# Kernel tuning notes

Measured on AMD Instinct MI355X. Metric: run time of the kernel, lower is better.

Reference implementation:

```python
import jax, jax.numpy as jnp
import numpy as np

XBOUND = (-51.2, 51.2, 0.8)
YBOUND = (-51.2, 51.2, 0.8)
ZBOUND = (-10.0, 10.0, 20.0)
DBOUND = (1.0, 60.0, 1.0)
IMG_H, IMG_W = 256, 704
DOWNSAMPLE = 16
CAM_C = 64
OUT_C = 64
D = int((DBOUND[1] - DBOUND[0]) / DBOUND[2])      # 59
NX = int((XBOUND[1] - XBOUND[0]) / XBOUND[2])     # 128
NY = int((YBOUND[1] - YBOUND[0]) / YBOUND[2])     # 128
NZ = int((ZBOUND[1] - ZBOUND[0]) / ZBOUND[2])     # 1
FH, FW = IMG_H // DOWNSAMPLE, IMG_W // DOWNSAMPLE # 16, 44
DX = jnp.array([XBOUND[2], YBOUND[2], ZBOUND[2]], dtype=jnp.float32)
BX = jnp.array([XBOUND[0] + XBOUND[2] / 2.0, YBOUND[0] + YBOUND[2] / 2.0, ZBOUND[0] + ZBOUND[2] / 2.0], dtype=jnp.float32)


def make_frustum():
    ds = jnp.arange(DBOUND[0], DBOUND[1], DBOUND[2], dtype=jnp.float32)   # [D]
    xs = jnp.linspace(0.0, IMG_W - 1.0, FW, dtype=jnp.float32)            # [FW]
    ys = jnp.linspace(0.0, IMG_H - 1.0, FH, dtype=jnp.float32)            # [FH]
    d = jnp.broadcast_to(ds[:, None, None], (D, FH, FW))
    x = jnp.broadcast_to(xs[None, None, :], (D, FH, FW))
    y = jnp.broadcast_to(ys[None, :, None], (D, FH, FW))
    return jnp.stack([x, y, d], axis=-1)                                  # [D,FH,FW,3]


def get_geometry(rots, trans, intrins, post_rots, post_trans):
    # rots/intrins/post_rots: [B,N,3,3]; trans/post_trans: [B,N,3]
    frustum = make_frustum()                                              # [D,FH,FW,3]
    pts = frustum[None, None] - post_trans[:, :, None, None, None]        # [B,N,D,FH,FW,3]
    pts = jnp.einsum('bnij,bndhwj->bndhwi', jnp.linalg.inv(post_rots), pts)
    pts = jnp.concatenate([pts[..., :2] * pts[..., 2:3], pts[..., 2:3]], axis=-1)
    comb = jnp.matmul(rots, jnp.linalg.inv(intrins))
    pts = jnp.einsum('bnij,bndhwj->bndhwi', comb, pts)
    return pts + trans[:, :, None, None, None]


def forward(x, rots, trans, intrins, post_rots, post_trans, w_depth, b_depth):
    B, N, C_in, H, W = x.shape
    # 1x1 conv == channel matmul
    y = jnp.einsum('bnchw,oc->bnohw', x, w_depth) + b_depth[None, None, :, None, None]
    depth = jax.nn.softmax(y[:, :, :D], axis=2)              # [B,N,D,H,W]
    context = y[:, :, D:]                                    # [B,N,OUT_C,H,W]
    outer = depth[:, :, :, None] * context[:, :, None, :]    # [B,N,D,OUT_C,H,W]
    outer = jnp.transpose(outer, (0, 1, 2, 4, 5, 3))         # [B,N,D,H,W,OUT_C]

    geom = jax.lax.stop_gradient(get_geometry(rots, trans, intrins, post_rots, post_trans))
    # torch .long() truncates toward zero -> jnp.trunc
    g = jnp.trunc((geom.reshape(-1, 3) - (BX - DX / 2.0)) / DX).astype(jnp.int32)  # [P,3]
    kept = ((g[:, 0] >= 0) & (g[:, 0] < NX) &
            (g[:, 1] >= 0) & (g[:, 1] < NY) &
            (g[:, 2] >= 0) & (g[:, 2] < NZ))
    batch_ix = jnp.repeat(jnp.arange(B, dtype=jnp.int32), N * D * H * W)
    ranks = batch_ix * (NX * NY * NZ) + g[:, 0] + g[:, 1] * NX + g[:, 2] * NX * NY
    # segment-sum over voxel ranks == sort+cumsum trick + scatter in the original
    feats = jnp.where(kept[:, None], outer.reshape(-1, OUT_C), 0.0)
    ranks = jnp.where(kept, ranks, 0)
    bev = jax.ops.segment_sum(feats, ranks, num_segments=B * NZ * NY * NX)
    bev = bev.reshape(B, NZ, NY, NX, OUT_C).transpose(0, 4, 1, 2, 3).sum(axis=2)
    return bev  # [B, OUT_C, NY, NX]


def setup_inputs() -> dict:
    key = jax.random.key(0)
    B, N = 4, 6
    ks = jax.random.split(key, 8)
    cam2ego = jnp.array([[0.0, 0.0, 1.0], [-1.0, 0.0, 0.0], [0.0, -1.0, 0.0]], dtype=jnp.float32)
    rots = jnp.broadcast_to(cam2ego, (B, N, 3, 3)) + 0.02 * jax.random.normal(ks[0], (B, N, 3, 3), dtype=jnp.float32)
    trans = 1.0 * jax.random.normal(ks[1], (B, N, 3), dtype=jnp.float32)
    K = jnp.array([[700.0, 0.0, IMG_W / 2.0], [0.0, 700.0, IMG_H / 2.0], [0.0, 0.0, 1.0]], dtype=jnp.float32)
    intrins = jnp.broadcast_to(K, (B, N, 3, 3)) + 0.1 * jax.random.normal(ks[2], (B, N, 3, 3), dtype=jnp.float32)
    post_rots = jnp.broadcast_to(jnp.eye(3, dtype=jnp.float32), (B, N, 3, 3)) + 0.01 * jax.random.normal(ks[3], (B, N, 3, 3), dtype=jnp.float32)
    post_trans = 0.1 * jax.random.normal(ks[4], (B, N, 3), dtype=jnp.float32)
    x = jax.random.normal(ks[5], (B, N, CAM_C, FH, FW), dtype=jnp.float32)
    w_depth = 0.05 * jax.random.normal(ks[6], (D + OUT_C, CAM_C), dtype=jnp.float32)
    b_depth = jnp.zeros((D + OUT_C,), dtype=jnp.float32)
    return {"x": x, "rots": rots, "trans": trans, "intrins": intrins,
            "post_rots": post_rots, "post_trans": post_trans,
            "w_depth": w_depth, "b_depth": b_depth}


def reference(x, rots, trans, intrins, post_rots, post_trans, w_depth, b_depth):
    return forward(x, rots, trans, intrins, post_rots, post_trans, w_depth, b_depth)
```

## Files before the change

kernel.cpp:

```cpp
#include <hip/hip_runtime.h>
#include <math.h>

#define Bc 4
#define Nc 6
#define Dc 59
#define FHc 16
#define FWc 44
#define Cc 64
#define OCc 123
#define NXc 128
#define NYc 128
#define NVOX (Bc*NXc*NYc)
#define NBLK (Bc*Nc*FWc)

#define WS_ACC 0
#define WS_CAM ((size_t)16777216)
#define WS_WDT ((size_t)16781312)

template<bool FMA>
__device__ __forceinline__ float mulsub(float a, float b, float c) {
    if (FMA) return __fmaf_rn(-a, b, c);
    return __fadd_rn(c, __fmul_rn(-a, b));
}

template<bool FMA>
__device__ __forceinline__ void lu_inv3x3T(const float* __restrict__ m, float* __restrict__ o) {
    float A[3][3] = {{m[0],m[3],m[6]},{m[1],m[4],m[7]},{m[2],m[5],m[8]}};
    int piv0, piv1;
    {
        float a0=fabsf(A[0][0]), a1=fabsf(A[1][0]), a2=fabsf(A[2][0]);
        int p = 0; float mx = a0;
        if (a1 > mx) { mx = a1; p = 1; }
        if (a2 > mx) { mx = a2; p = 2; }
        piv0 = p;
        if (p != 0) { for (int k=0;k<3;++k){ float t=A[0][k]; A[0][k]=A[p][k]; A[p][k]=t; } }
        const float d = __fdiv_rn(1.0f, A[0][0]);
        A[1][0] = __fmul_rn(A[1][0], d);
        A[2][0] = __fmul_rn(A[2][0], d);
        #pragma unroll
        for (int i=1;i<3;++i)
            #pragma unroll
            for (int j=1;j<3;++j)
                A[i][j] = mulsub<FMA>(A[i][0], A[0][j], A[i][j]);
    }
    {
        float a1=fabsf(A[1][1]), a2=fabsf(A[2][1]);
        int p = (a2 > a1) ? 2 : 1;
        piv1 = p;
        if (p != 1) { for (int k=0;k<3;++k){ float t=A[1][k]; A[1][k]=A[p][k]; A[p][k]=t; } }
        const float d = __fdiv_rn(1.0f, A[1][1]);
        A[2][1] = __fmul_rn(A[2][1], d);
        A[2][2] = mulsub<FMA>(A[2][1], A[1][2], A[2][2]);
    }
    float B[3][3] = {{1.f,0.f,0.f},{0.f,1.f,0.f},{0.f,0.f,1.f}};
    if (piv0 != 0) { for (int k=0;k<3;++k){ float t=B[0][k]; B[0][k]=B[piv0][k]; B[piv0][k]=t; } }
    if (piv1 != 1) { for (int k=0;k<3;++k){ float t=B[1][k]; B[1][k]=B[piv1][k]; B[piv1][k]=t; } }
    #pragma unroll
    for (int j=0;j<3;++j) {
        B[1][j] = mulsub<FMA>(A[1][0], B[0][j], B[1][j]);
        B[2][j] = mulsub<FMA>(A[2][0], B[0][j], B[2][j]);
        B[2][j] = mulsub<FMA>(A[2][1], B[1][j], B[2][j]);
        B[2][j] = __fdiv_rn(B[2][j], A[2][2]);
        B[0][j] = mulsub<FMA>(A[0][2], B[2][j], B[0][j]);
        B[1][j] = mulsub<FMA>(A[1][2], B[2][j], B[1][j]);
        B[1][j] = __fdiv_rn(B[1][j], A[1][1]);
        B[0][j] = mulsub<FMA>(A[0][1], B[1][j], B[0][j]);
        B[0][j] = __fdiv_rn(B[0][j], A[0][0]);
    }
    o[0]=B[0][0]; o[1]=B[1][0]; o[2]=B[2][0];
    o[3]=B[0][1]; o[4]=B[1][1]; o[5]=B[2][1];
    o[6]=B[0][2]; o[7]=B[1][2]; o[8]=B[2][2];
}

template<bool FMA>
__device__ __forceinline__ float dot3(float a0,float a1,float a2,float b0,float b1,float b2){
    if (FMA) return __fmaf_rn(a2,b2, __fmaf_rn(a1,b1, __fmul_rn(a0,b0)));
    return __fadd_rn(__fadd_rn(__fmul_rn(a0,b0), __fmul_rn(a1,b1)), __fmul_rn(a2,b2));
}

__global__ __launch_bounds__(256) void prep(
    const float* __restrict__ wd, const float* __restrict__ rots,
    const float* __restrict__ intrins, const float* __restrict__ post_rots,
    float* __restrict__ wdT2, float* __restrict__ camMat, float4* __restrict__ acc4)
{
    const int gid = blockIdx.x*256 + threadIdx.x;
    const float4 z = make_float4(0.f, 0.f, 0.f, 0.f);
    acc4[gid] = z;
    acc4[gid + 524288] = z;

    if (gid < OCc*Cc) {
        const int o = gid >> 6, c = gid & 63;
        const int slot = (o < 64) ? (o << 1) : (((o - 64) << 1) | 1);
        wdT2[(c << 7) + slot] = wd[gid];
    } else if (gid < OCc*Cc + 320) {
        const int k = gid - OCc*Cc;
        const int c = k / 5, o = 59 + (k % 5);
        wdT2[(c << 7) + (o << 1) + 1] = 0.0f;
    }
    if (gid < 48) {
        const int cam = gid >> 1;
        const int var = gid & 1;
        const float* pr = post_rots + cam*9;
        const float* ro = rots      + cam*9;
        const float* it = intrins   + cam*9;
        float PRi[9], INi[9], CM[9];
        if (var == 0) { lu_inv3x3T<true >(pr, PRi); lu_inv3x3T<true >(it, INi); }
        else          { lu_inv3x3T<false>(pr, PRi); lu_inv3x3T<false>(it, INi); }
        #pragma unroll
        for (int r2 = 0; r2 < 3; ++r2)
            #pragma unroll
            for (int c2 = 0; c2 < 3; ++c2)
                CM[r2*3+c2] = dot3<true>(ro[r2*3+0], ro[r2*3+1], ro[r2*3+2],
                                         INi[0*3+c2], INi[1*3+c2], INi[2*3+c2]);
        float* dst = camMat + (size_t)(cam*2 + var)*18;
        #pragma unroll
        for (int k = 0; k < 9; ++k) { dst[k] = PRi[k]; dst[9+k] = CM[k]; }
    }
}

template<bool FMA>
__device__ __forceinline__ int geom_light(
    const float* __restrict__ PRi, const float* __restrict__ CM,
    float pt0, float pt1, float pt2, float tr0, float tr1, float tr2,
    float u, float v, float dval, int b)
{
    const float p0 = __fsub_rn(u,    pt0);
    const float p1 = __fsub_rn(v,    pt1);
    const float p2 = __fsub_rn(dval, pt2);
    const float q0 = dot3<FMA>(PRi[0],PRi[1],PRi[2], p0,p1,p2);
    const float q1 = dot3<FMA>(PRi[3],PRi[4],PRi[5], p0,p1,p2);
    const float q2 = dot3<FMA>(PRi[6],PRi[7],PRi[8], p0,p1,p2);
    const float r0 = __fmul_rn(q0, q2);
    const float r1 = __fmul_rn(q1, q2);
    const float s0 = __fadd_rn(dot3<FMA>(CM[0],CM[1],CM[2], r0,r1,q2), tr0);
    const float s1 = __fadd_rn(dot3<FMA>(CM[3],CM[4],CM[5], r0,r1,q2), tr1);
    const float s2 = __fadd_rn(dot3<FMA>(CM[6],CM[7],CM[8], r0,r1,q2), tr2);
    const float CX  = -51.200000762939453f;
    const float DXf =  0.80000001192092896f;
    const float gx = __fdiv_rn(__fsub_rn(s0, CX), DXf);
    const float gy = __fdiv_rn(__fsub_rn(s1, CX), DXf);
    const float gz = __fdiv_rn(__fsub_rn(s2, -10.0f), 20.0f);
    const bool kept = (gx > -1.0f) && (gx < 128.0f) &&
                      (gy > -1.0f) && (gy < 128.0f) &&
                      (gz > -1.0f) && (gz < 1.0f);
    return kept ? (b*(NXc*NYc) + ((int)gy)*NXc + (int)gx) : -1;
}

__global__ __launch_bounds__(512, 8) void lss_main(
    const float* __restrict__ x, const float* __restrict__ trans,
    const float* __restrict__ post_trans, const float* __restrict__ bd,
    const float* __restrict__ wdT2, const float* __restrict__ camMat,
    float* __restrict__ acc)
{
    const int blk = blockIdx.x;
    const int wi  = blk % FWc;
    const int cam = blk / FWc;
    const int b   = cam / Nc;
    const int t = threadIdx.x;
    const int wave = t >> 6, lane = t & 63;

    __shared__ float  xsT[64][16];
    __shared__ float  yv[16][60];
    __shared__ float  ctxT[64][18];
    __shared__ float4 geo[Dc][16];

    {
        const float* xb = x + (size_t)cam*64*(FHc*FWc) + wi;
        for (int idx = t; idx < 1024; idx += 512) {
            const int c = idx >> 4, hi = idx & 15;
            xsT[c][hi] = xb[(size_t)c*(FHc*FWc) + hi*FWc];
        }
    }
    __syncthreads();

    {
        const int hi0 = wave << 1;
        float a0[2] = {0.f,0.f}, a1[2] = {0.f,0.f};
        const float2* wrow = (const float2*)wdT2 + lane;
        #pragma unroll 8
        for (int c = 0; c < 64; ++c) {
            const float2 wv = wrow[c << 6];
            const float2 xv = *(const float2*)&xsT[c][hi0];
            a0[0] = __fmaf_rn(wv.x, xv.x, a0[0]); a1[0] = __fmaf_rn(wv.y, xv.x, a1[0]);
            a0[1] = __fmaf_rn(wv.x, xv.y, a0[1]); a1[1] = __fmaf_rn(wv.y, xv.y, a1[1]);
        }
        const float b0 = bd[lane];
        const float b1 = (lane < 59) ? bd[64 + lane] : 0.0f;
        #pragma unroll
        for (int k = 0; k < 2; ++k) {
            const int hi = hi0 + k;
            const float y0 = __fadd_rn(a0[k], b0);
            if (lane < 59) {
                yv[hi][lane] = y0;
                ctxT[lane + 5][hi] = __fadd_rn(a1[k], b1);
            } else {
                ctxT[lane - 59][hi] = y0;
            }
        }
    }
    for (int k = 0; k < 2; ++k) {
        const int hi = (wave << 1) | k;
        float v = (lane < Dc) ? yv[hi][lane] : -INFINITY;
        float m = v;
        #pragma unroll
        for (int off = 32; off; off >>= 1) m = fmaxf(m, __shfl_xor(m, off));
        float e = (lane < Dc) ? expf(__fsub_rn(v, m)) : 0.0f;
        float s = e;
        #pragma unroll
        for (int off = 32; off; off >>= 1) s = __fadd_rn(s, __shfl_xor(s, off));
        if (lane < Dc) yv[hi][lane] = __fdiv_rn(e, s);
    }
    __syncthreads();

    {
        const float pt0 = post_trans[cam*3+0], pt1 = post_trans[cam*3+1], pt2 = post_trans[cam*3+2];
        const float tr0 = trans[cam*3+0],      tr1 = trans[cam*3+1],      tr2 = trans[cam*3+2];
        const float* M0 = camMat + (size_t)(cam*2 + 0)*18;
        const float* M1 = camMat + (size_t)(cam*2 + 1)*18;
        const float u = (float)(wi * (703.0 / 43.0));
        for (int idx = t; idx < 16*Dc; idx += 512) {
            const int d = idx >> 4, hi = idx & 15;
            const float v    = (float)(hi * 17.0);
            const float dval = (float)(1 + d);
            const int vA = geom_light<true >(M0, M0+9, pt0,pt1,pt2, tr0,tr1,tr2, u, v, dval, b);
            const int vB = geom_light<false>(M1, M1+9, pt0,pt1,pt2, tr0,tr1,tr2, u, v, dval, b);
            geo[d][hi] = make_float4(yv[hi][d], __int_as_float(vA), __int_as_float(vB), 0.0f);
        }
    }
    __syncthreads();

    {
        float cx[16];
        #pragma unroll
        for (int h = 0; h < 16; h += 2) {
            const float2 c2 = *(const float2*)&ctxT[lane][h];
            cx[h] = c2.x; cx[h+1] = c2.y;
        }
        for (int d = wave; d < Dc; d += 8) {
            int runVox = -1;
            float accv = 0.0f;
            #pragma unroll
            for (int hi = 0; hi < 16; ++hi) {
                const float4 g = geo[d][hi];
                const float dw = g.x;
                const int vA = __float_as_int(g.y);
                const int vB = __float_as_int(g.z);
                const float cxv = cx[hi];
                if (vA == vB) {
                    if (vA >= 0) {
                        if (vA != runVox) {
                            if (runVox >= 0) atomicAdd(&acc[((size_t)runVox << 6) + lane], accv);
                            runVox = vA; accv = 0.0f;
                        }
                        accv = __fadd_rn(accv, __fmul_rn(dw, cxv));
                    }
                } else {
                    const float hw = __fmul_rn(dw, 0.5f);
                    if (vA >= 0) {
                        if (vA != runVox) {
                            if (runVox >= 0) atomicAdd(&acc[((size_t)runVox << 6) + lane], accv);
                            runVox = vA; accv = 0.0f;
                        }
                        accv = __fadd_rn(accv, __fmul_rn(hw, cxv));
                    }
                    if (vB >= 0) atomicAdd(&acc[((size_t)vB << 6) + lane], __fmul_rn(hw, cxv));
                }
            }
            if (runVox >= 0) atomicAdd(&acc[((size_t)runVox << 6) + lane], accv);
        }
    }
}

__global__ __launch_bounds__(256) void lss_transpose(
    const float* __restrict__ acc, float* __restrict__ out)
{
    __shared__ float tile[64][65];
    const int blk = blockIdx.x;
    const int b = blk >> 8;
    const int pixbase = (blk & 255) * 64;
    const float4* src4 = (const float4*)(acc + ((size_t)b*16384 + pixbase)*64);
    const int t = threadIdx.x;
    #pragma unroll
    for (int i = 0; i < 4; ++i) {
        const int e4 = i*256 + t;
        const float4 v = src4[e4];
        const int e = e4 << 2;
        const int r = e & 63, c = e >> 6;
        tile[r+0][c] = v.x; tile[r+1][c] = v.y; tile[r+2][c] = v.z; tile[r+3][c] = v.w;
    }
    __syncthreads();
    float* dst = out + (size_t)b*64*16384 + pixbase;
    #pragma unroll
    for (int i = 0; i < 4; ++i) {
        const int idx = i*256 + t;
        const int c = idx >> 4, p = (idx & 15) << 2;
        const float4 v = make_float4(tile[c][p], tile[c][p+1], tile[c][p+2], tile[c][p+3]);
        *(float4*)&dst[(size_t)c*16384 + p] = v;
    }
}

extern "C" void kernel_launch(void* const* d_in, const int* in_sizes, int n_in,
                              void* d_out, int out_size, void* d_ws, size_t ws_size,
                              hipStream_t stream) {
    const float* x          = (const float*)d_in[0];
    const float* rots       = (const float*)d_in[1];
    const float* trans      = (const float*)d_in[2];
    const float* intrins    = (const float*)d_in[3];
    const float* post_rots  = (const float*)d_in[4];
    const float* post_trans = (const float*)d_in[5];
    const float* wd         = (const float*)d_in[6];
    const float* bd         = (const float*)d_in[7];
    float* out = (float*)d_out;
    char* ws = (char*)d_ws;

    float* acc    = (float*)(ws + WS_ACC);
    float* camMat = (float*)(ws + WS_CAM);
    float* wdT2   = (float*)(ws + WS_WDT);

    prep<<<dim3(2048), dim3(256), 0, stream>>>(
        wd, rots, intrins, post_rots, wdT2, camMat, (float4*)acc);
    lss_main<<<dim3(NBLK), dim3(512), 0, stream>>>(
        x, trans, post_trans, bd, wdT2, camMat, acc);
    lss_transpose<<<dim3(Bc*256), dim3(256), 0, stream>>>(acc, out);
}
```

Before: 185.0 us.

## Process two image columns per block with interleaved points for longer voxel runs

Measured after the change: 311.3 us. +68.3%, slower.

```diff
diff --git a/kernel.cpp b/kernel.cpp
--- a/kernel.cpp
+++ b/kernel.cpp
@@ -11,7 +11,7 @@
 #define NXc 128
 #define NYc 128
 #define NVOX (Bc*NXc*NYc)
-#define NBLK (Bc*Nc*FWc)
+#define NBLKM (Bc*Nc*(FWc/2))
 
 #define WS_ACC 0
 #define WS_CAM ((size_t)16777216)
@@ -146,41 +146,43 @@
     return kept ? (b*(NXc*NYc) + ((int)gy)*NXc + (int)gx) : -1;
 }
 
-__global__ __launch_bounds__(512, 8) void lss_main(
+__global__ __launch_bounds__(1024, 8) void lss_main(
     const float* __restrict__ x, const float* __restrict__ trans,
     const float* __restrict__ post_trans, const float* __restrict__ bd,
     const float* __restrict__ wdT2, const float* __restrict__ camMat,
     float* __restrict__ acc)
 {
     const int blk = blockIdx.x;
-    const int wi  = blk % FWc;
-    const int cam = blk / FWc;
+    const int wig = blk % (FWc/2);
+    const int cam = blk / (FWc/2);
+    const int wi0 = wig*2;
     const int b   = cam / Nc;
     const int t = threadIdx.x;
     const int wave = t >> 6, lane = t & 63;
 
-    __shared__ float  xsT[64][16];
-    __shared__ float  yv[16][60];
-    __shared__ float  ctxT[64][18];
-    __shared__ float4 geo[Dc][16];
-
-    {
-        const float* xb = x + (size_t)cam*64*(FHc*FWc) + wi;
-        for (int idx = t; idx < 1024; idx += 512) {
-            const int c = idx >> 4, hi = idx & 15;
-            xsT[c][hi] = xb[(size_t)c*(FHc*FWc) + hi*FWc];
+    __shared__ float  xsT[64][32];
+    __shared__ float  yv[32][60];
+    __shared__ float  ctxT[64][34];
+    __shared__ float4 geo[Dc][32];
+
+    {
+        const float* xb = x + (size_t)cam*64*(FHc*FWc);
+        for (int idx = t; idx < 2048; idx += 1024) {
+            const int c = idx >> 5, wj = idx & 31;
+            const int j = wj >> 4, hi = wj & 15;
+            xsT[c][wj] = xb[(size_t)c*(FHc*FWc) + hi*FWc + (wi0 + j)];
         }
     }
     __syncthreads();
 
     {
-        const int hi0 = wave << 1;
+        const int wj0 = wave << 1;
         float a0[2] = {0.f,0.f}, a1[2] = {0.f,0.f};
         const float2* wrow = (const float2*)wdT2 + lane;
         #pragma unroll 8
         for (int c = 0; c < 64; ++c) {
             const float2 wv = wrow[c << 6];
-            const float2 xv = *(const float2*)&xsT[c][hi0];
+            const float2 xv = *(const float2*)&xsT[c][wj0];
             a0[0] = __fmaf_rn(wv.x, xv.x, a0[0]); a1[0] = __fmaf_rn(wv.y, xv.x, a1[0]);
             a0[1] = __fmaf_rn(wv.x, xv.y, a0[1]); a1[1] = __fmaf_rn(wv.y, xv.y, a1[1]);
         }
@@ -188,19 +190,21 @@
         const float b1 = (lane < 59) ? bd[64 + lane] : 0.0f;
         #pragma unroll
         for (int k = 0; k < 2; ++k) {
-            const int hi = hi0 + k;
+            const int wj = wj0 + k;
+            const int j = wj >> 4, hi = wj & 15;
+            const int cwj = (hi << 1) | j;
             const float y0 = __fadd_rn(a0[k], b0);
             if (lane < 59) {
-                yv[hi][lane] = y0;
-                ctxT[lane + 5][hi] = __fadd_rn(a1[k], b1);
+                yv[wj][lane] = y0;
+                ctxT[lane + 5][cwj] = __fadd_rn(a1[k], b1);
             } else {
-                ctxT[lane - 59][hi] = y0;
+                ctxT[lane - 59][cwj] = y0;
             }
         }
     }
     for (int k = 0; k < 2; ++k) {
-        const int hi = (wave << 1) | k;
-        float v = (lane < Dc) ? yv[hi][lane] : -INFINITY;
+        const int wj = (wave << 1) | k;
+        float v = (lane < Dc) ? yv[wj][lane] : -INFINITY;
         float m = v;
         #pragma unroll
         for (int off = 32; off; off >>= 1) m = fmaxf(m, __shfl_xor(m, off));
@@ -208,7 +212,7 @@
         float s = e;
         #pragma unroll
         for (int off = 32; off; off >>= 1) s = __fadd_rn(s, __shfl_xor(s, off));
-        if (lane < Dc) yv[hi][lane] = __fdiv_rn(e, s);
+        if (lane < Dc) yv[wj][lane] = __fdiv_rn(e, s);
     }
     __syncthreads();
 
@@ -217,57 +221,55 @@
         const float tr0 = trans[cam*3+0],      tr1 = trans[cam*3+1],      tr2 = trans[cam*3+2];
         const float* M0 = camMat + (size_t)(cam*2 + 0)*18;
         const float* M1 = camMat + (size_t)(cam*2 + 1)*18;
-        const float u = (float)(wi * (703.0 / 43.0));
-        for (int idx = t; idx < 16*Dc; idx += 512) {
-            const int d = idx >> 4, hi = idx & 15;
+        for (int idx = t; idx < 32*Dc; idx += 1024) {
+            const int d = idx >> 5, cwj = idx & 31;
+            const int j = cwj & 1, hi = cwj >> 1;
+            const float u    = (float)((wi0 + j) * (703.0 / 43.0));
             const float v    = (float)(hi * 17.0);
             const float dval = (float)(1 + d);
             const int vA = geom_light<true >(M0, M0+9, pt0,pt1,pt2, tr0,tr1,tr2, u, v, dval, b);
             const int vB = geom_light<false>(M1, M1+9, pt0,pt1,pt2, tr0,tr1,tr2, u, v, dval, b);
-            geo[d][hi] = make_float4(yv[hi][d], __int_as_float(vA), __int_as_float(vB), 0.0f);
+            geo[d][cwj] = make_float4(yv[(j<<4)|hi][d], __int_as_float(vA), __int_as_float(vB), 0.0f);
         }
     }
     __syncthreads();
 
-    {
-        float cx[16];
-        #pragma unroll
-        for (int h = 0; h < 16; h += 2) {
-            const float2 c2 = *(const float2*)&ctxT[lane][h];
-            cx[h] = c2.x; cx[h+1] = c2.y;
-        }
-        for (int d = wave; d < Dc; d += 8) {
-            int runVox = -1;
-            float accv = 0.0f;
-            #pragma unroll
-            for (int hi = 0; hi < 16; ++hi) {
-                const float4 g = geo[d][hi];
-                const float dw = g.x;
-                const int vA = __float_as_int(g.y);
-                const int vB = __float_as_int(g.z);
-                const float cxv = cx[hi];
-                if (vA == vB) {
-                    if (vA >= 0) {
-                        if (vA != runVox) {
-                            if (runVox >= 0) atomicAdd(&acc[((size_t)runVox << 6) + lane], accv);
-                            runVox = vA; accv = 0.0f;
-                        }
-                        accv = __fadd_rn(accv, __fmul_rn(dw, cxv));
+    for (int d = wave; d < Dc; d += 16) {
+        int runVox = -1;
+        float accv = 0.0f;
+        float cx0 = 0.0f, cx1 = 0.0f;
+        #pragma unroll
+        for (int cwj = 0; cwj < 32; ++cwj) {
+            if ((cwj & 1) == 0) {
+                const float2 c2 = *(const float2*)&ctxT[lane][cwj];
+                cx0 = c2.x; cx1 = c2.y;
+            }
+            const float cxv = (cwj & 1) ? cx1 : cx0;
+            const float4 g = geo[d][cwj];
+            const float dw = g.x;
+            const int vA = __float_as_int(g.y);
+            const int vB = __float_as_int(g.z);
+            if (vA == vB) {
+                if (vA >= 0) {
+                    if (vA != runVox) {
+                        if (runVox >= 0) atomicAdd(&acc[((size_t)runVox << 6) + lane], accv);
+                        runVox = vA; accv = 0.0f;
                     }
-                } else {
-                    const float hw = __fmul_rn(dw, 0.5f);
-                    if (vA >= 0) {
-                        if (vA != runVox) {
-                            if (runVox >= 0) atomicAdd(&acc[((size_t)runVox << 6) + lane], accv);
-                            runVox = vA; accv = 0.0f;
-                        }
-                        accv = __fadd_rn(accv, __fmul_rn(hw, cxv));
+                    accv = __fadd_rn(accv, __fmul_rn(dw, cxv));
+                }
+            } else {
+                const float hw = __fmul_rn(dw, 0.5f);
+                if (vA >= 0) {
+                    if (vA != runVox) {
+                        if (runVox >= 0) atomicAdd(&acc[((size_t)runVox << 6) + lane], accv);
+                        runVox = vA; accv = 0.0f;
                     }
-                    if (vB >= 0) atomicAdd(&acc[((size_t)vB << 6) + lane], __fmul_rn(hw, cxv));
+                    accv = __fadd_rn(accv, __fmul_rn(hw, cxv));
                 }
+                if (vB >= 0) atomicAdd(&acc[((size_t)vB << 6) + lane], __fmul_rn(hw, cxv));
             }
-            if (runVox >= 0) atomicAdd(&acc[((size_t)runVox << 6) + lane], accv);
-        }
+        }
+        if (runVox >= 0) atomicAdd(&acc[((size_t)runVox << 6) + lane], accv);
     }
 }
 
@@ -319,7 +321,7 @@
 
     prep<<<dim3(2048), dim3(256), 0, stream>>>(
         wd, rots, intrins, post_rots, wdT2, camMat, (float4*)acc);
-    lss_main<<<dim3(NBLK), dim3(512), 0, stream>>>(
+    lss_main<<<dim3(NBLKM), dim3(1024), 0, stream>>>(
         x, trans, post_trans, bd, wdT2, camMat, acc);
     lss_transpose<<<dim3(Bc*256), dim3(256), 0, stream>>>(acc, out);
 }
```

## Group frustum points by voxel in a shared-memory hash table before atomics

Applied to the files above, without the earlier changes.

After: 202.0 us. 9.2% more time.

```diff
diff --git a/kernel.cpp b/kernel.cpp
--- a/kernel.cpp
+++ b/kernel.cpp
@@ -12,6 +12,9 @@
 #define NYc 128
 #define NVOX (Bc*NXc*NYc)
 #define NBLK (Bc*Nc*FWc)
+#define NREC (16*Dc)
+#define NSLOT 512
+#define NENT 2048
 
 #define WS_ACC 0
 #define WS_CAM ((size_t)16777216)
@@ -159,10 +162,14 @@
     const int t = threadIdx.x;
     const int wave = t >> 6, lane = t & 63;
 
-    __shared__ float  xsT[64][16];
-    __shared__ float  yv[16][60];
-    __shared__ float  ctxT[64][18];
-    __shared__ float4 geo[Dc][16];
+    __shared__ float xsT[64][16];
+    __shared__ float yv[16][60];
+    __shared__ float ctxT[64][18];
+    __shared__ int   slotVox[NSLOT];
+    __shared__ int   slotHead[NSLOT];
+    __shared__ unsigned short nxt[NENT];
+    __shared__ unsigned short meta[NENT];
+    __shared__ int   nEntries;
 
     {
         const float* xb = x + (size_t)cam*64*(FHc*FWc) + wi;
@@ -170,6 +177,8 @@
             const int c = idx >> 4, hi = idx & 15;
             xsT[c][hi] = xb[(size_t)c*(FHc*FWc) + hi*FWc];
         }
+        if (t < NSLOT) { slotVox[t] = -1; slotHead[t] = -1; }
+        if (t == 0) nEntries = 0;
     }
     __syncthreads();
 
@@ -218,13 +227,36 @@
         const float* M0 = camMat + (size_t)(cam*2 + 0)*18;
         const float* M1 = camMat + (size_t)(cam*2 + 1)*18;
         const float u = (float)(wi * (703.0 / 43.0));
-        for (int idx = t; idx < 16*Dc; idx += 512) {
+        for (int idx = t; idx < NREC; idx += 512) {
             const int d = idx >> 4, hi = idx & 15;
             const float v    = (float)(hi * 17.0);
             const float dval = (float)(1 + d);
             const int vA = geom_light<true >(M0, M0+9, pt0,pt1,pt2, tr0,tr1,tr2, u, v, dval, b);
             const int vB = geom_light<false>(M1, M1+9, pt0,pt1,pt2, tr0,tr1,tr2, u, v, dval, b);
-            geo[d][hi] = make_float4(yv[hi][d], __int_as_float(vA), __int_as_float(vB), 0.0f);
+            const int split = (vA != vB);
+            #pragma unroll
+            for (int s2 = 0; s2 < 2; ++s2) {
+                const int vox = s2 ? vB : vA;
+                if (vox < 0 || (!split && s2)) continue;
+                int slot = (int)(((unsigned)vox * 2654435761u) >> 16) & (NSLOT-1);
+                int probes = 0;
+                while (true) {
+                    int old = atomicCAS(&slotVox[slot], -1, vox);
+                    if (old == -1 || old == vox) break;
+                    slot = (slot + 1) & (NSLOT-1);
+                    if (++probes >= NSLOT) { slot = -1; break; }
+                }
+                if (slot >= 0) {
+                    const int e = atomicAdd(&nEntries, 1);
+                    meta[e] = (unsigned short)((d << 5) | (hi << 1) | split);
+                    nxt[e]  = (unsigned short)atomicExch(&slotHead[slot], e);
+                } else {
+                    const float dep = yv[hi][d];
+                    const float w = split ? __fmul_rn(dep, 0.5f) : dep;
+                    for (int ch = 0; ch < 64; ++ch)
+                        atomicAdd(&acc[((size_t)vox << 6) + ch], __fmul_rn(w, ctxT[ch][hi]));
+                }
+            }
         }
     }
     __syncthreads();
@@ -236,37 +268,22 @@
             const float2 c2 = *(const float2*)&ctxT[lane][h];
             cx[h] = c2.x; cx[h+1] = c2.y;
         }
-        for (int d = wave; d < Dc; d += 8) {
-            int runVox = -1;
+        for (int slot = wave; slot < NSLOT; slot += 8) {
+            const int vox = slotVox[slot];
+            if (vox < 0) continue;
             float accv = 0.0f;
-            #pragma unroll
-            for (int hi = 0; hi < 16; ++hi) {
-                const float4 g = geo[d][hi];
-                const float dw = g.x;
-                const int vA = __float_as_int(g.y);
-                const int vB = __float_as_int(g.z);
-                const float cxv = cx[hi];
-                if (vA == vB) {
-                    if (vA >= 0) {
-                        if (vA != runVox) {
-                            if (runVox >= 0) atomicAdd(&acc[((size_t)runVox << 6) + lane], accv);
-                            runVox = vA; accv = 0.0f;
-                        }
-                        accv = __fadd_rn(accv, __fmul_rn(dw, cxv));
-                    }
-                } else {
-                    const float hw = __fmul_rn(dw, 0.5f);
-                    if (vA >= 0) {
-                        if (vA != runVox) {
-                            if (runVox >= 0) atomicAdd(&acc[((size_t)runVox << 6) + lane], accv);
-                            runVox = vA; accv = 0.0f;
-                        }
-                        accv = __fadd_rn(accv, __fmul_rn(hw, cxv));
-                    }
-                    if (vB >= 0) atomicAdd(&acc[((size_t)vB << 6) + lane], __fmul_rn(hw, cxv));
-                }
+            int e = slotHead[slot];
+            while (e >= 0) {
+                const unsigned short m = meta[e];
+                const int d  = m >> 5;
+                const int hi = (m >> 1) & 15;
+                const float dep = yv[hi][d];
+                const float w = (m & 1) ? __fmul_rn(dep, 0.5f) : dep;
+                accv = __fadd_rn(accv, __fmul_rn(w, cx[hi]));
+                const unsigned short nx = nxt[e];
+                e = (nx == 0xFFFFu) ? -1 : (int)nx;
             }
-            if (runVox >= 0) atomicAdd(&acc[((size_t)runVox << 6) + lane], accv);
+            atomicAdd(&acc[((size_t)vox << 6) + lane], accv);
         }
     }
 }
```
